# Optimization experiments

Measured on AMD Instinct MI355X. Metric: run time of the kernel, lower is better.

The kernel has to match this reference:

```python
import jax, jax.numpy as jnp
import numpy as np

D = 1024
H = 16
HD = D // H

def setup_inputs() -> dict:
    key = jax.random.key(0)
    ks = jax.random.split(key, 8)
    scale = 1.0 / np.sqrt(D)
    x = jax.random.normal(ks[0], (2, 2048, D), dtype=jnp.float32)
    Wq = jax.random.uniform(ks[1], (D, D), jnp.float32, -scale, scale)
    bq = jax.random.uniform(ks[2], (D,), jnp.float32, -scale, scale)
    Wk = jax.random.uniform(ks[3], (D, D), jnp.float32, -scale, scale)
    bk = jax.random.uniform(ks[4], (D,), jnp.float32, -scale, scale)
    Wv = jax.random.uniform(ks[5], (D, D), jnp.float32, -scale, scale)
    bv = jax.random.uniform(ks[6], (D,), jnp.float32, -scale, scale)
    B = jnp.zeros((1, H, 1, 1), dtype=jnp.float32)
    return {"x": x, "Wq": Wq, "bq": bq, "Wk": Wk, "bk": bk, "Wv": Wv, "bv": bv, "B": B}

def reference(x, Wq, bq, Wk, bk, Wv, bv, B):
    bsz, seq, _ = x.shape
    def proj(W, b):
        # [b, s, D] -> [b, h, s, hd]
        y = x @ W.T + b
        return y.reshape(bsz, seq, H, HD).transpose(0, 2, 1, 3)
    q = proj(Wq, bq)
    k = proj(Wk, bk)
    v = proj(Wv, bv)
    scores = jnp.einsum('bhqd,bhkd->bhqk', q, k) / np.sqrt(HD) + B
    attn = jax.nn.softmax(scores, axis=-1)
    out = jnp.einsum('bhqk,bhkd->bhqd', attn, v)
    return out.transpose(0, 2, 1, 3).reshape(bsz, seq, D)
```

## Files before the change

kernel.cpp:

```cpp
#include <hip/hip_runtime.h>
#include <stdint.h>

typedef __attribute__((ext_vector_type(8))) short s8v;
typedef __attribute__((ext_vector_type(4))) short s4v;
typedef __attribute__((ext_vector_type(4))) float f4v;

#define D_DIM 1024
#define H_NUM 16
#define HD 64
#define SEQ 2048
#define BSZ 2
#define MROWS (BSZ * SEQ)
#define LOG2E 1.4426950408889634f

__device__ __forceinline__ unsigned short f2bf(float f) {
  unsigned u = __builtin_bit_cast(unsigned, f);
  u += 0x7fffu + ((u >> 16) & 1u);
  return (unsigned short)(u >> 16);
}

__device__ __forceinline__ float exp2q(float x) {
  float r;
  asm("v_exp_f32 %0, %1" : "=v"(r) : "v"(x));
  return r;
}

__device__ __forceinline__ float max3q(float a, float b, float c) {
  float r;
  asm("v_max3_f32 %0, %1, %2, %3" : "=v"(r) : "v"(a), "v"(b), "v"(c));
  return r;
}

__device__ __forceinline__ unsigned int cvtpk(float a, float b) {
  unsigned int r;
  asm("v_cvt_pk_bf16_f32 %0, %1, %2" : "=v"(r) : "v"(a), "v"(b));
  return r;
}

__device__ __forceinline__ void async16(const unsigned short* g, unsigned short* l) {
  __builtin_amdgcn_global_load_lds(
      (__attribute__((address_space(1))) unsigned int*)(uintptr_t)g,
      (__attribute__((address_space(3))) unsigned int*)l, 16, 0, 0);
}

__device__ __forceinline__ f4v mfma16(s8v a, s8v b, f4v c) {
  return __builtin_amdgcn_mfma_f32_16x16x32_bf16(a, b, c, 0, 0, 0);
}

__device__ __forceinline__ void barrier_raw() {
  __builtin_amdgcn_sched_barrier(0);
  __builtin_amdgcn_s_barrier();
  __builtin_amdgcn_sched_barrier(0);
}
#define WAITVM0() asm volatile("s_waitcnt vmcnt(0)" ::: "memory")

__global__ __launch_bounds__(256) void cvt_all(
    const float* __restrict__ x, const float* __restrict__ Wq,
    const float* __restrict__ Wk, const float* __restrict__ Wv,
    unsigned short* __restrict__ Xb, unsigned short* __restrict__ Wb) {
  const int NX = MROWS * D_DIM / 4;
  const int NW = D_DIM * D_DIM / 4;
  int i = blockIdx.x * 256 + threadIdx.x;
  const float* src;
  unsigned short* dst;
  int off;
  if (i < NX) {
    src = x; dst = Xb; off = i;
  } else if (i < NX + NW) {
    src = Wq; dst = Wb; off = i - NX;
  } else if (i < NX + 2 * NW) {
    src = Wk; dst = Wb + D_DIM * D_DIM; off = i - NX - NW;
  } else {
    src = Wv; dst = Wb + 2 * D_DIM * D_DIM; off = i - NX - 2 * NW;
  }
  f4v v = *(const f4v*)(src + (size_t)off * 4);
  s4v o;
  o[0] = (short)f2bf(v[0]);
  o[1] = (short)f2bf(v[1]);
  o[2] = (short)f2bf(v[2]);
  o[3] = (short)f2bf(v[3]);
  *(s4v*)(dst + (size_t)off * 4) = o;
}

__global__ __launch_bounds__(256) void qkv_gemm(
    const unsigned short* __restrict__ Xb, const unsigned short* __restrict__ Wb,
    const float* __restrict__ bq, const float* __restrict__ bk,
    const float* __restrict__ bv, unsigned short* __restrict__ qb,
    unsigned short* __restrict__ kb, unsigned short* __restrict__ vt) {
  __shared__ __align__(16) unsigned short At[2][128 * 32];
  __shared__ __align__(16) unsigned short Bt[2][128 * 32];

  const int z = blockIdx.z;
  const unsigned short* W = Wb + z * (D_DIM * D_DIM);
  const float* bias = (z == 0) ? bq : ((z == 1) ? bk : bv);
  const int row0 = blockIdx.x * 128;
  const int col0 = blockIdx.y * 128;
  const int t = threadIdx.x;
  const int w = t >> 6, l = t & 63;
  const int wr = w >> 1, wc = w & 1;
  const int lg = l >> 4, lc = l & 15;

  f4v acc[4][4];
#pragma unroll
  for (int m = 0; m < 4; ++m)
#pragma unroll
    for (int n = 0; n < 4; ++n) acc[m][n] = (f4v){0.f, 0.f, 0.f, 0.f};

  const int srow = t >> 2;
  const int sch = (t & 3) ^ ((t >> 3) & 3);
  const unsigned short* Asrc = Xb + (size_t)(row0 + srow) * D_DIM + sch * 8;
  const unsigned short* Bsrc = W + (size_t)(col0 + srow) * D_DIM + sch * 8;

  const int rch = lg ^ ((lc >> 1) & 3);
  const int arow = wr * 64 + lc;
  const int brow = wc * 64 + lc;

#define STAGE(b, k0)                                                        \
  do {                                                                      \
    async16(Asrc + (k0), At[b] + t * 8);                                    \
    async16(Asrc + (k0) + 64 * D_DIM, At[b] + 2048 + t * 8);                \
    async16(Bsrc + (k0), Bt[b] + t * 8);                                    \
    async16(Bsrc + (k0) + 64 * D_DIM, Bt[b] + 2048 + t * 8);                \
  } while (0)

  STAGE(0, 0);
  WAITVM0();
  barrier_raw();

  int cur = 0;
  for (int it = 0; it < 32; ++it) {
    if (it < 31) STAGE(cur ^ 1, (it + 1) * 32);
    s8v a[4], b[4];
#pragma unroll
    for (int m = 0; m < 4; ++m)
      a[m] = *(const s8v*)(At[cur] + (arow + m * 16) * 32 + rch * 8);
#pragma unroll
    for (int n = 0; n < 4; ++n)
      b[n] = *(const s8v*)(Bt[cur] + (brow + n * 16) * 32 + rch * 8);
    __builtin_amdgcn_s_setprio(1);
#pragma unroll
    for (int m = 0; m < 4; ++m)
#pragma unroll
      for (int n = 0; n < 4; ++n) acc[m][n] = mfma16(a[m], b[n], acc[m][n]);
    __builtin_amdgcn_s_setprio(0);
    WAITVM0();
    barrier_raw();
    cur ^= 1;
  }
#undef STAGE

  const float SCQ = 0.125f * LOG2E;
#pragma unroll
  for (int m = 0; m < 4; ++m) {
    const int sg0 = row0 + wr * 64 + m * 16 + 4 * lg;
    const int b = sg0 >> 11;
    const int sl0 = sg0 & (SEQ - 1);
#pragma unroll
    for (int n = 0; n < 4; ++n) {
      const int j = col0 + wc * 64 + n * 16 + lc;
      const int h = j >> 6, hd = j & 63;
      const float bs = bias[j];
      if (z == 2) {
        s4v o;
#pragma unroll
        for (int r = 0; r < 4; ++r) o[r] = (short)f2bf(acc[m][n][r] + bs);
        *(s4v*)(vt + ((size_t)(b * H_NUM + h) * HD + hd) * SEQ + sl0) = o;
      } else if (z == 0) {
#pragma unroll
        for (int r = 0; r < 4; ++r)
          qb[((size_t)(b * H_NUM + h) * SEQ + (sl0 + r)) * HD + hd] =
              f2bf((acc[m][n][r] + bs) * SCQ);
      } else {
#pragma unroll
        for (int r = 0; r < 4; ++r)
          kb[((size_t)(b * H_NUM + h) * SEQ + (sl0 + r)) * HD + hd] =
              f2bf(acc[m][n][r] + bs);
      }
    }
  }
}

__global__ __launch_bounds__(512, 4) void attn_fwd(
    const unsigned short* __restrict__ qb, const unsigned short* __restrict__ kb,
    const unsigned short* __restrict__ vt, const float* __restrict__ Bb,
    float* __restrict__ out) {
  __shared__ __align__(16) unsigned short Kl[2][64 * 64];
  __shared__ __align__(16) unsigned short Vl[2][64 * 64];
  __shared__ __align__(16) unsigned short Pl[8][16 * 64];

  const int bh = blockIdx.x;
  const int b = bh >> 4, h = bh & 15;
  const int q0 = blockIdx.y * 128;
  const int t = threadIdx.x, w = t >> 6, l = t & 63;
  const int lg = l >> 4, lc = l & 15;
  const int swz = lc & 7;
  (void)Bb;

  const unsigned short* Q = qb + (size_t)bh * SEQ * HD;
  const unsigned short* K = kb + (size_t)bh * SEQ * HD;
  const unsigned short* V = vt + (size_t)bh * HD * SEQ;

  const int qrow = q0 + w * 16 + lc;
  s8v qf0 = *(const s8v*)(Q + (size_t)qrow * HD + 8 * lg);
  s8v qf1 = *(const s8v*)(Q + (size_t)qrow * HD + 32 + 8 * lg);

  s8v ones;
#pragma unroll
  for (int i = 0; i < 8; ++i) ones[i] = (short)0x3F80;

  f4v acc[4];
#pragma unroll
  for (int n = 0; n < 4; ++n) acc[n] = (f4v){0.f, 0.f, 0.f, 0.f};
  f4v lacc = (f4v){0.f, 0.f, 0.f, 0.f};
  float m = -3.0e38f, thr = -3.0e38f;

  const int srow = t >> 3;
  const int sc8 = (t & 7) ^ (srow & 7);
  const unsigned short* Kst = K + (size_t)srow * HD + sc8 * 8;
  const unsigned short* Vst = V + (size_t)srow * SEQ + sc8 * 8;
  unsigned short* Kd = Kl[0] + t * 8;
  unsigned short* Vd = Vl[0] + t * 8;
  const int ldsw = 64 * 64;

#define STAGE_KV(bsel)                                                      \
  do {                                                                      \
    async16(Kst, Kd + (bsel) * ldsw);                                       \
    async16(Vst, Vd + (bsel) * ldsw);                                       \
    Kst += 64 * HD;                                                         \
    Vst += 64;                                                              \
  } while (0)

  const int kfo0 = lc * 64 + (lg ^ swz) * 8;
  const int kfo1 = lc * 64 + ((4 + lg) ^ swz) * 8;
  unsigned short* const Pw = Pl[w];
  const unsigned short* pbr0 = Pw + lc * 64 + ((0 + lg) ^ swz) * 8;
  const unsigned short* pbr1 = Pw + lc * 64 + ((4 + lg) ^ swz) * 8;
  unsigned short* pwr[4];
#pragma unroll
  for (int kt4 = 0; kt4 < 4; ++kt4)
    pwr[kt4] = Pw + lc * 64 + (((2 * kt4 + (lg >> 1)) ^ swz) * 8) + 4 * (lg & 1);

  STAGE_KV(0);
  WAITVM0();
  barrier_raw();

  int cur = 0;
  for (int kt = 0; kt < SEQ / 64; ++kt) {
    if (kt < SEQ / 64 - 1) STAGE_KV(cur ^ 1);

    const unsigned short* Kb_ = Kl[cur];
    const unsigned short* Vb_ = Vl[cur];

    f4v sv[4];
    __builtin_amdgcn_s_setprio(1);
#pragma unroll
    for (int kt4 = 0; kt4 < 4; ++kt4) {
      s8v kf0 = *(const s8v*)(Kb_ + kfo0 + kt4 * 1024);
      s8v kf1 = *(const s8v*)(Kb_ + kfo1 + kt4 * 1024);
      f4v c = (f4v){0.f, 0.f, 0.f, 0.f};
      c = mfma16(kf0, qf0, c);
      c = mfma16(kf1, qf1, c);
      sv[kt4] = c;
    }
    __builtin_amdgcn_s_setprio(0);

    float t0 = max3q(sv[0][0], sv[0][1], sv[0][2]);
    float t1 = max3q(sv[0][3], sv[1][0], sv[1][1]);
    float t2 = max3q(sv[1][2], sv[1][3], sv[2][0]);
    float t3 = max3q(sv[2][1], sv[2][2], sv[2][3]);
    float t4 = max3q(sv[3][0], sv[3][1], sv[3][2]);
    float tmax = fmaxf(max3q(t0, t1, sv[3][3]), max3q(t2, t3, t4));

    if (!__all(tmax <= thr)) {
      float tr = tmax;
      tr = fmaxf(tr, __shfl_xor(tr, 16));
      tr = fmaxf(tr, __shfl_xor(tr, 32));
      const float mn = fmaxf(m, tr);
      const float fs = exp2q(m - mn);
      m = mn;
      thr = mn + 8.0f;
#pragma unroll
      for (int n = 0; n < 4; ++n)
#pragma unroll
        for (int r = 0; r < 4; ++r) acc[n][r] *= fs;
#pragma unroll
      for (int r = 0; r < 4; ++r) lacc[r] *= fs;
    }

#pragma unroll
    for (int kt4 = 0; kt4 < 4; ++kt4) {
#pragma unroll
      for (int r = 0; r < 4; ++r) sv[kt4][r] = exp2q(sv[kt4][r] - m);
      uint2 dw;
      dw.x = cvtpk(sv[kt4][0], sv[kt4][1]);
      dw.y = cvtpk(sv[kt4][2], sv[kt4][3]);
      *(uint2*)pwr[kt4] = dw;
    }

    __builtin_amdgcn_s_setprio(1);
    {
      s8v pb0 = *(const s8v*)pbr0;
      s8v pb1 = *(const s8v*)pbr1;
      lacc = mfma16(ones, pb0, lacc);
      lacc = mfma16(ones, pb1, lacc);
#pragma unroll
      for (int n = 0; n < 4; ++n) {
        s8v vf0 = *(const s8v*)(Vb_ + kfo0 + n * 1024);
        s8v vf1 = *(const s8v*)(Vb_ + kfo1 + n * 1024);
        acc[n] = mfma16(vf0, pb0, acc[n]);
        acc[n] = mfma16(vf1, pb1, acc[n]);
      }
    }
    __builtin_amdgcn_s_setprio(0);

    WAITVM0();
    barrier_raw();
    cur ^= 1;
  }
#undef STAGE_KV

  const float inv = 1.0f / lacc[0];
  const int q = q0 + w * 16 + lc;
#pragma unroll
  for (int n = 0; n < 4; ++n) {
    f4v o;
#pragma unroll
    for (int r = 0; r < 4; ++r) o[r] = acc[n][r] * inv;
    *(f4v*)(out + ((size_t)(b * SEQ + q)) * D_DIM + h * 64 + n * 16 + 4 * lg) = o;
  }
}

extern "C" void kernel_launch(void* const* d_in, const int* in_sizes, int n_in,
                              void* d_out, int out_size, void* d_ws, size_t ws_size,
                              hipStream_t stream) {
  const float* x = (const float*)d_in[0];
  const float* Wq = (const float*)d_in[1];
  const float* bq = (const float*)d_in[2];
  const float* Wk = (const float*)d_in[3];
  const float* bk = (const float*)d_in[4];
  const float* Wv = (const float*)d_in[5];
  const float* bv = (const float*)d_in[6];
  const float* Bb = (const float*)d_in[7];
  float* out = (float*)d_out;

  char* ws = (char*)d_ws;
  unsigned short* Xb = (unsigned short*)ws;
  unsigned short* Wb = (unsigned short*)(ws + (8ull << 20));
  unsigned short* qb = (unsigned short*)(ws + (14ull << 20));
  unsigned short* kb = (unsigned short*)(ws + (22ull << 20));
  unsigned short* vt = (unsigned short*)(ws + (30ull << 20));

  cvt_all<<<7168, 256, 0, stream>>>(x, Wq, Wk, Wv, Xb, Wb);

  dim3 ggrid(MROWS / 128, D_DIM / 128, 3);
  qkv_gemm<<<ggrid, 256, 0, stream>>>(Xb, Wb, bq, bk, bv, qb, kb, vt);

  dim3 agrid(BSZ * H_NUM, SEQ / 128);
  attn_fwd<<<agrid, 512, 0, stream>>>(qb, kb, vt, Bb, out);
}
```

Baseline: 92.90 us.

## Switch attention to 32x32 MFMA with register-resident P via permlane swaps

Rewrites the attention kernel to use 32x32x16 bf16 MFMAs, with each of 4 waves owning 32 query rows instead of 8 waves owning 16. The P matrix stays in registers, rearranged with v_permlane32_swap instead of a round trip through LDS. The row sum is accumulated with VALU adds instead of an extra MFMA against a ones vector. This removes the P LDS traffic and the ones-MFMA at the cost of more registers per wave and fewer waves per block.

```diff
diff --git a/kernel.cpp b/kernel.cpp
--- a/kernel.cpp
+++ b/kernel.cpp
@@ -4,6 +4,7 @@
 typedef __attribute__((ext_vector_type(8))) short s8v;
 typedef __attribute__((ext_vector_type(4))) short s4v;
 typedef __attribute__((ext_vector_type(4))) float f4v;
+typedef __attribute__((ext_vector_type(16))) float f16v;
 
 #define D_DIM 1024
 #define H_NUM 16
@@ -45,6 +46,10 @@
 
 __device__ __forceinline__ f4v mfma16(s8v a, s8v b, f4v c) {
   return __builtin_amdgcn_mfma_f32_16x16x32_bf16(a, b, c, 0, 0, 0);
+}
+
+__device__ __forceinline__ f16v mfma32(s8v a, s8v b, f16v c) {
+  return __builtin_amdgcn_mfma_f32_32x32x16_bf16(a, b, c, 0, 0, 0);
 }
 
 __device__ __forceinline__ void barrier_raw() {
@@ -180,39 +185,41 @@
   }
 }
 
-__global__ __launch_bounds__(512, 4) void attn_fwd(
+__global__ __launch_bounds__(256) void attn_fwd(
     const unsigned short* __restrict__ qb, const unsigned short* __restrict__ kb,
     const unsigned short* __restrict__ vt, const float* __restrict__ Bb,
     float* __restrict__ out) {
   __shared__ __align__(16) unsigned short Kl[2][64 * 64];
   __shared__ __align__(16) unsigned short Vl[2][64 * 64];
-  __shared__ __align__(16) unsigned short Pl[8][16 * 64];
 
   const int bh = blockIdx.x;
   const int b = bh >> 4, h = bh & 15;
   const int q0 = blockIdx.y * 128;
   const int t = threadIdx.x, w = t >> 6, l = t & 63;
-  const int lg = l >> 4, lc = l & 15;
-  const int swz = lc & 7;
+  const int ql = l & 31, hi = l >> 5;
   (void)Bb;
 
   const unsigned short* Q = qb + (size_t)bh * SEQ * HD;
   const unsigned short* K = kb + (size_t)bh * SEQ * HD;
   const unsigned short* V = vt + (size_t)bh * HD * SEQ;
 
-  const int qrow = q0 + w * 16 + lc;
-  s8v qf0 = *(const s8v*)(Q + (size_t)qrow * HD + 8 * lg);
-  s8v qf1 = *(const s8v*)(Q + (size_t)qrow * HD + 32 + 8 * lg);
-
-  s8v ones;
-#pragma unroll
-  for (int i = 0; i < 8; ++i) ones[i] = (short)0x3F80;
-
-  f4v acc[4];
-#pragma unroll
-  for (int n = 0; n < 4; ++n) acc[n] = (f4v){0.f, 0.f, 0.f, 0.f};
-  f4v lacc = (f4v){0.f, 0.f, 0.f, 0.f};
-  float m = -3.0e38f, thr = -3.0e38f;
+  const int qrow = q0 + w * 32 + ql;
+  const unsigned short* Qp = Q + (size_t)qrow * HD + 8 * hi;
+  s8v qf[4];
+#pragma unroll
+  for (int ks = 0; ks < 4; ++ks) qf[ks] = *(const s8v*)(Qp + ks * 16);
+
+  f16v acc0, acc1;
+#pragma unroll
+  for (int i = 0; i < 16; ++i) { acc0[i] = 0.f; acc1[i] = 0.f; }
+  float m = -3.0e38f, thr = -3.0e38f, lsum = 0.f;
+
+  int off0[4], off1[4];
+#pragma unroll
+  for (int ks = 0; ks < 4; ++ks) {
+    off0[ks] = ql * 64 + (((2 * ks + hi) ^ (ql & 7)) * 8);
+    off1[ks] = off0[ks] + 2048;
+  }
 
   const int srow = t >> 3;
   const int sc8 = (t & 7) ^ (srow & 7);
@@ -225,21 +232,13 @@
 #define STAGE_KV(bsel)                                                      \
   do {                                                                      \
     async16(Kst, Kd + (bsel) * ldsw);                                       \
+    async16(Kst + 32 * HD, Kd + (bsel) * ldsw + 2048);                      \
     async16(Vst, Vd + (bsel) * ldsw);                                       \
+    async16(Vst + 32 * SEQ, Vd + (bsel) * ldsw + 2048);                     \
     Kst += 64 * HD;                                                         \
     Vst += 64;                                                              \
   } while (0)
 
-  const int kfo0 = lc * 64 + (lg ^ swz) * 8;
-  const int kfo1 = lc * 64 + ((4 + lg) ^ swz) * 8;
-  unsigned short* const Pw = Pl[w];
-  const unsigned short* pbr0 = Pw + lc * 64 + ((0 + lg) ^ swz) * 8;
-  const unsigned short* pbr1 = Pw + lc * 64 + ((4 + lg) ^ swz) * 8;
-  unsigned short* pwr[4];
-#pragma unroll
-  for (int kt4 = 0; kt4 < 4; ++kt4)
-    pwr[kt4] = Pw + lc * 64 + (((2 * kt4 + (lg >> 1)) ^ swz) * 8) + 4 * (lg & 1);
-
   STAGE_KV(0);
   WAITVM0();
   barrier_raw();
@@ -251,65 +250,89 @@
     const unsigned short* Kb_ = Kl[cur];
     const unsigned short* Vb_ = Vl[cur];
 
-    f4v sv[4];
+    f16v s0, s1;
+#pragma unroll
+    for (int i = 0; i < 16; ++i) { s0[i] = 0.f; s1[i] = 0.f; }
     __builtin_amdgcn_s_setprio(1);
 #pragma unroll
-    for (int kt4 = 0; kt4 < 4; ++kt4) {
-      s8v kf0 = *(const s8v*)(Kb_ + kfo0 + kt4 * 1024);
-      s8v kf1 = *(const s8v*)(Kb_ + kfo1 + kt4 * 1024);
-      f4v c = (f4v){0.f, 0.f, 0.f, 0.f};
-      c = mfma16(kf0, qf0, c);
-      c = mfma16(kf1, qf1, c);
-      sv[kt4] = c;
+    for (int ks = 0; ks < 4; ++ks) {
+      s8v kf0 = *(const s8v*)(Kb_ + off0[ks]);
+      s8v kf1 = *(const s8v*)(Kb_ + off1[ks]);
+      s0 = mfma32(kf0, qf[ks], s0);
+      s1 = mfma32(kf1, qf[ks], s1);
     }
     __builtin_amdgcn_s_setprio(0);
 
-    float t0 = max3q(sv[0][0], sv[0][1], sv[0][2]);
-    float t1 = max3q(sv[0][3], sv[1][0], sv[1][1]);
-    float t2 = max3q(sv[1][2], sv[1][3], sv[2][0]);
-    float t3 = max3q(sv[2][1], sv[2][2], sv[2][3]);
-    float t4 = max3q(sv[3][0], sv[3][1], sv[3][2]);
-    float tmax = fmaxf(max3q(t0, t1, sv[3][3]), max3q(t2, t3, t4));
+    float a0 = max3q(s0[0], s0[1], s0[2]);
+    float a1 = max3q(s0[3], s0[4], s0[5]);
+    float a2 = max3q(s0[6], s0[7], s0[8]);
+    float a3 = max3q(s0[9], s0[10], s0[11]);
+    float a4 = max3q(s0[12], s0[13], s0[14]);
+    float a5 = max3q(s0[15], s1[0], s1[1]);
+    float a6 = max3q(s1[2], s1[3], s1[4]);
+    float a7 = max3q(s1[5], s1[6], s1[7]);
+    float a8 = max3q(s1[8], s1[9], s1[10]);
+    float a9 = max3q(s1[11], s1[12], s1[13]);
+    float b0 = max3q(a0, a1, a2);
+    float b1 = max3q(a3, a4, a5);
+    float b2 = max3q(a6, a7, a8);
+    float b3 = max3q(a9, s1[14], s1[15]);
+    float tmax = fmaxf(fmaxf(b0, b1), fmaxf(b2, b3));
 
     if (!__all(tmax <= thr)) {
-      float tr = tmax;
-      tr = fmaxf(tr, __shfl_xor(tr, 16));
-      tr = fmaxf(tr, __shfl_xor(tr, 32));
+      float tr = fmaxf(tmax, __shfl_xor(tmax, 32));
       const float mn = fmaxf(m, tr);
       const float fs = exp2q(m - mn);
       m = mn;
       thr = mn + 8.0f;
 #pragma unroll
-      for (int n = 0; n < 4; ++n)
-#pragma unroll
-        for (int r = 0; r < 4; ++r) acc[n][r] *= fs;
-#pragma unroll
-      for (int r = 0; r < 4; ++r) lacc[r] *= fs;
-    }
-
-#pragma unroll
-    for (int kt4 = 0; kt4 < 4; ++kt4) {
-#pragma unroll
-      for (int r = 0; r < 4; ++r) sv[kt4][r] = exp2q(sv[kt4][r] - m);
-      uint2 dw;
-      dw.x = cvtpk(sv[kt4][0], sv[kt4][1]);
-      dw.y = cvtpk(sv[kt4][2], sv[kt4][3]);
-      *(uint2*)pwr[kt4] = dw;
+      for (int i = 0; i < 16; ++i) { acc0[i] *= fs; acc1[i] *= fs; }
+      lsum *= fs;
+    }
+
+#pragma unroll
+    for (int i = 0; i < 16; ++i) {
+      s0[i] = exp2q(s0[i] - m);
+      s1[i] = exp2q(s1[i] - m);
+    }
+    {
+      float p0 = (s0[0] + s0[1]) + (s0[2] + s0[3]);
+      float p1 = (s0[4] + s0[5]) + (s0[6] + s0[7]);
+      float p2 = (s0[8] + s0[9]) + (s0[10] + s0[11]);
+      float p3 = (s0[12] + s0[13]) + (s0[14] + s0[15]);
+      float p4 = (s1[0] + s1[1]) + (s1[2] + s1[3]);
+      float p5 = (s1[4] + s1[5]) + (s1[6] + s1[7]);
+      float p6 = (s1[8] + s1[9]) + (s1[10] + s1[11]);
+      float p7 = (s1[12] + s1[13]) + (s1[14] + s1[15]);
+      lsum += ((p0 + p1) + (p2 + p3)) + ((p4 + p5) + (p6 + p7));
+    }
+
+    unsigned int u[16];
+#pragma unroll
+    for (int x = 0; x < 8; ++x) {
+      u[x] = cvtpk(s0[2 * x], s0[2 * x + 1]);
+      u[8 + x] = cvtpk(s1[2 * x], s1[2 * x + 1]);
+    }
+    s8v pb[4];
+#pragma unroll
+    for (int ks = 0; ks < 4; ++ks) {
+      const int base = (ks >> 1) * 8 + (ks & 1) * 4;
+      unsigned int x0 = u[base + 0], y0 = u[base + 2];
+      unsigned int x1 = u[base + 1], y1 = u[base + 3];
+      asm("v_permlane32_swap_b32 %0, %1" : "+v"(x0), "+v"(y0));
+      asm("v_permlane32_swap_b32 %0, %1" : "+v"(x1), "+v"(y1));
+      union { s8v v; unsigned int w[4]; } bb;
+      bb.w[0] = x0; bb.w[1] = x1; bb.w[2] = y0; bb.w[3] = y1;
+      pb[ks] = bb.v;
     }
 
     __builtin_amdgcn_s_setprio(1);
-    {
-      s8v pb0 = *(const s8v*)pbr0;
-      s8v pb1 = *(const s8v*)pbr1;
-      lacc = mfma16(ones, pb0, lacc);
-      lacc = mfma16(ones, pb1, lacc);
-#pragma unroll
-      for (int n = 0; n < 4; ++n) {
-        s8v vf0 = *(const s8v*)(Vb_ + kfo0 + n * 1024);
-        s8v vf1 = *(const s8v*)(Vb_ + kfo1 + n * 1024);
-        acc[n] = mfma16(vf0, pb0, acc[n]);
-        acc[n] = mfma16(vf1, pb1, acc[n]);
-      }
+#pragma unroll
+    for (int ks = 0; ks < 4; ++ks) {
+      s8v vf0 = *(const s8v*)(Vb_ + off0[ks]);
+      s8v vf1 = *(const s8v*)(Vb_ + off1[ks]);
+      acc0 = mfma32(vf0, pb[ks], acc0);
+      acc1 = mfma32(vf1, pb[ks], acc1);
     }
     __builtin_amdgcn_s_setprio(0);
 
@@ -319,14 +342,20 @@
   }
 #undef STAGE_KV
 
-  const float inv = 1.0f / lacc[0];
-  const int q = q0 + w * 16 + lc;
-#pragma unroll
-  for (int n = 0; n < 4; ++n) {
-    f4v o;
-#pragma unroll
-    for (int r = 0; r < 4; ++r) o[r] = acc[n][r] * inv;
-    *(f4v*)(out + ((size_t)(b * SEQ + q)) * D_DIM + h * 64 + n * 16 + 4 * lg) = o;
+  lsum += __shfl_xor(lsum, 32);
+  const float inv = 1.0f / lsum;
+  const int q = q0 + w * 32 + ql;
+  float* op = out + ((size_t)(b * SEQ + q)) * D_DIM + h * 64;
+#pragma unroll
+  for (int g = 0; g < 4; ++g) {
+    f4v o0, o1;
+#pragma unroll
+    for (int r = 0; r < 4; ++r) {
+      o0[r] = acc0[4 * g + r] * inv;
+      o1[r] = acc1[4 * g + r] * inv;
+    }
+    *(f4v*)(op + 8 * g + 4 * hi) = o0;
+    *(f4v*)(op + 32 + 8 * g + 4 * hi) = o1;
   }
 }
 
@@ -356,5 +385,5 @@
   qkv_gemm<<<ggrid, 256, 0, stream>>>(Xb, Wb, bq, bk, bv, qb, kb, vt);
 
   dim3 agrid(BSZ * H_NUM, SEQ / 128);
-  attn_fwd<<<agrid, 512, 0, stream>>>(qb, kb, vt, Bb, out);
-}
+  attn_fwd<<<agrid, 256, 0, stream>>>(qb, kb, vt, Bb, out);
+}
```

Result: slower. 96.27 us (+3.6%).
